# Kernel tuning notes

Hardware: AMD Instinct MI355X
Metric: run time of the kernel (lower is better)

Reference implementation:

```python
import jax, jax.numpy as jnp
import numpy as np

BITS = 4
MAXQ = (1 << BITS) - 1
PACK = 32 // BITS  # values packed per int32
GROUP_SIZE = 128


def dequant_weight(qweight, qzeros, scales, g_idx):
    """GPTQ tritonv2-style dequant: W[i,j] = (w_int[i,j] - z_int[g_idx[i],j]) * scales[g_idx[i],j]."""
    in_features = qweight.shape[0] * PACK
    out_features = qweight.shape[1]
    rows = jnp.arange(in_features)
    # unpack along infeatures: row i lives in qweight[i//PACK], nibble (i%PACK)
    w_int = (qweight[rows // PACK] >> ((rows % PACK) * BITS)[:, None]) & MAXQ  # [in, out]
    cols = jnp.arange(out_features)
    # unpack zeros along outfeatures
    z_int = (qzeros[:, cols // PACK] >> ((cols % PACK) * BITS)[None, :]) & MAXQ  # [groups, out]
    dt = scales.dtype
    return (w_int.astype(dt) - z_int.astype(dt)[g_idx]) * scales[g_idx]  # [in, out]


def setup_inputs() -> dict:
    key = jax.random.key(0)
    k1, k2, k3, k4, k5 = jax.random.split(key, 5)
    B, S, IN, OUT = 4, 2048, 4096, 11008
    groups = IN // GROUP_SIZE
    x = jax.random.normal(k1, (B, S, IN), dtype=jnp.float32)
    qweight = jax.random.randint(k2, (IN // PACK, OUT), 0, 2147483647, dtype=jnp.int32)
    qzeros = jax.random.randint(k3, (groups, OUT // PACK), 0, 2147483647, dtype=jnp.int32)
    scales = jax.random.uniform(k4, (groups, OUT), dtype=jnp.float32, minval=0.001, maxval=0.02)
    g_idx = (jnp.arange(IN) // GROUP_SIZE).astype(jnp.int32)
    bias = jax.random.normal(k5, (OUT,), dtype=jnp.float32) * 0.01
    return {"x": x, "qweight": qweight, "qzeros": qzeros, "scales": scales, "g_idx": g_idx, "bias": bias}


def reference(x, qweight, qzeros, scales, g_idx, bias):
    W = dequant_weight(qweight, qzeros, scales, g_idx)  # [in, out]
    out = x.reshape(-1, x.shape[-1]) @ W + bias  # [tokens, out]
    return out.reshape(x.shape[:-1] + (W.shape[1],)).astype(x.dtype)
```

## Files before the change

kernel.cpp:

```cpp
#include <hip/hip_runtime.h>

typedef __bf16 bf16x8 __attribute__((ext_vector_type(8)));
typedef __bf16 bf16x4 __attribute__((ext_vector_type(4)));
typedef float  f32x4  __attribute__((ext_vector_type(4)));

constexpr int BM  = 128;
constexpr int BN  = 128;
constexpr int BK  = 64;
constexpr int LDK = 72;

__global__ __launch_bounds__(256, 2)
void gptq_gemm_fused(const float* __restrict__ X,
                     const unsigned int* __restrict__ QW,
                     const unsigned int* __restrict__ QZ,
                     const float* __restrict__ SC,
                     const float* __restrict__ BIAS,
                     float* __restrict__ OUT,
                     const int M, const int N, const int K)
{
    __shared__ __bf16 As[BM * LDK];
    __shared__ __bf16 Bs[BN * LDK];

    const int tid = threadIdx.x;
    const int nTn = N / BN;
    const int m0  = (blockIdx.x / nTn) * BM;
    const int n0  = (blockIdx.x % nTn) * BN;

    const int lane = tid & 63;
    const int wave = tid >> 6;
    const int wm   = (wave >> 1) * 64;
    const int wn   = (wave & 1) * 64;
    const int l15  = lane & 15;
    const int lk8  = (lane >> 4) * 8;

    const int a_kc = (tid & 15) * 4;
    const int a_r0 = tid >> 4;
    const int b_c  = tid & 127;
    const int b_r0 = tid >> 7;
    const int N8   = N >> 3;

    f32x4 acc[4][4] = {};

    float4 av[8];
    unsigned int bw[4];
    float scale, nzs;

    auto load_tile = [&](int kt_) {
        const int k0 = kt_ * BK;
        #pragma unroll
        for (int i = 0; i < 8; ++i)
            av[i] = *(const float4*)&X[(m0 + a_r0 + 16 * i) * K + k0 + a_kc];
        const int qr = k0 >> 3;
        #pragma unroll
        for (int i = 0; i < 4; ++i)
            bw[i] = QW[(qr + b_r0 + 2 * i) * N + n0 + b_c];
        const int g = k0 >> 7;
        scale = SC[g * N + n0 + b_c];
        const unsigned int qzv = QZ[g * N8 + ((n0 + b_c) >> 3)];
        const int z = (qzv >> (((n0 + b_c) & 7) * 4)) & 15;
        nzs = (float)z * scale;
    };

    load_tile(0);

    const int kTiles = K / BK;
    for (int kt = 0; kt < kTiles; ++kt) {
        __syncthreads();

        #pragma unroll
        for (int i = 0; i < 8; ++i) {
            bf16x4 v = { (__bf16)av[i].x, (__bf16)av[i].y,
                         (__bf16)av[i].z, (__bf16)av[i].w };
            *(bf16x4*)&As[(a_r0 + 16 * i) * LDK + a_kc] = v;
        }
        {
            const float s = scale, nz = nzs;
            #pragma unroll
            for (int i = 0; i < 4; ++i) {
                const unsigned int w32 = bw[i];
                bf16x8 v;
                #pragma unroll
                for (int j = 0; j < 8; ++j) {
                    const int w = (w32 >> (4 * j)) & 15;
                    v[j] = (__bf16)((float)w * s - nz);
                }
                *(bf16x8*)&Bs[b_c * LDK + (b_r0 + 2 * i) * 8] = v;
            }
        }
        __syncthreads();

        if (kt + 1 < kTiles) load_tile(kt + 1);

        #pragma unroll
        for (int ks = 0; ks < 2; ++ks) {
            bf16x8 af[4], bfr[4];
            #pragma unroll
            for (int mi = 0; mi < 4; ++mi)
                af[mi] = *(bf16x8*)&As[(wm + mi * 16 + l15) * LDK + ks * 32 + lk8];
            #pragma unroll
            for (int ni = 0; ni < 4; ++ni)
                bfr[ni] = *(bf16x8*)&Bs[(wn + ni * 16 + l15) * LDK + ks * 32 + lk8];
            #pragma unroll
            for (int mi = 0; mi < 4; ++mi)
                #pragma unroll
                for (int ni = 0; ni < 4; ++ni)
                    acc[mi][ni] = __builtin_amdgcn_mfma_f32_16x16x32_bf16(
                        af[mi], bfr[ni], acc[mi][ni], 0, 0, 0);
        }
    }

    const int cb = n0 + wn + l15;
    const int rb = m0 + wm + (lane >> 4) * 4;
    #pragma unroll
    for (int ni = 0; ni < 4; ++ni) {
        const float bv = BIAS[cb + ni * 16];
        #pragma unroll
        for (int mi = 0; mi < 4; ++mi) {
            #pragma unroll
            for (int r = 0; r < 4; ++r)
                OUT[(size_t)(rb + mi * 16 + r) * N + cb + ni * 16] = acc[mi][ni][r] + bv;
        }
    }
}

extern "C" void kernel_launch(void* const* d_in, const int* in_sizes, int n_in,
                              void* d_out, int out_size, void* d_ws, size_t ws_size,
                              hipStream_t stream) {
    const float*        x    = (const float*)d_in[0];
    const unsigned int* qw   = (const unsigned int*)d_in[1];
    const unsigned int* qz   = (const unsigned int*)d_in[2];
    const float*        sc   = (const float*)d_in[3];
    const float*        bias = (const float*)d_in[5];
    float*              out  = (float*)d_out;

    const int K = in_sizes[4];
    const int N = in_sizes[5];
    const int M = in_sizes[0] / K;

    const dim3 grid((M / BM) * (N / BN));
    gptq_gemm_fused<<<grid, 256, 0, stream>>>(x, qw, qz, sc, bias, out, M, N, K);
}
```

Before: 1.373 ms.

## Split into bf16 pre-conversion, dequant-transpose, and async-LDS GEMM kernels

Replaces the single fused kernel with three kernels when workspace allows. The first converts X to bf16, the second dequantizes the weights into a transposed bf16 matrix through XOR-swizzled LDS, and the third is a GEMM that loads tiles directly into LDS with global_load_lds under a swizzled layout and a grouped block order. This removes the per-tile float-to-bf16 conversion and repeated dequantization from the GEMM inner loop, and halves the activation bytes the GEMM reads. The cost is extra workspace traffic to write and reread the bf16 X and W copies, and the GEMM still has no double buffering.

New measurement: 1.306 ms. -4.9%, faster.

```diff
diff --git a/kernel.cpp b/kernel.cpp
--- a/kernel.cpp
+++ b/kernel.cpp
@@ -3,6 +3,147 @@
 typedef __bf16 bf16x8 __attribute__((ext_vector_type(8)));
 typedef __bf16 bf16x4 __attribute__((ext_vector_type(4)));
 typedef float  f32x4  __attribute__((ext_vector_type(4)));
+
+typedef __attribute__((address_space(3))) unsigned int        lds_u32_t;
+typedef const __attribute__((address_space(1))) unsigned int  glob_u32_t;
+
+__global__ __launch_bounds__(256)
+void cvt_x_bf16(const float* __restrict__ X, __bf16* __restrict__ XB, long long n8)
+{
+    long long i = (long long)blockIdx.x * 256 + threadIdx.x;
+    if (i >= n8) return;
+    const float4* src = (const float4*)X + 2 * i;
+    float4 a = src[0], b = src[1];
+    bf16x8 v = { (__bf16)a.x, (__bf16)a.y, (__bf16)a.z, (__bf16)a.w,
+                 (__bf16)b.x, (__bf16)b.y, (__bf16)b.z, (__bf16)b.w };
+    *(bf16x8*)(XB + 8 * i) = v;
+}
+
+__global__ __launch_bounds__(256)
+void dequant_wt(const unsigned int* __restrict__ QW,
+                const unsigned int* __restrict__ QZ,
+                const float* __restrict__ SC,
+                __bf16* __restrict__ WT,
+                const int N, const int K)
+{
+    __shared__ __bf16 T[256 * 64];
+    const int tid = threadIdx.x;
+    const int nK  = K >> 6;
+    const int n0  = (blockIdx.x / nK) * 256;
+    const int k0  = (blockIdx.x % nK) * 64;
+
+    const int n = n0 + tid;
+    const int g = k0 >> 7;
+    const float s = SC[g * N + n];
+    const unsigned int qzv = QZ[g * (N >> 3) + (n >> 3)];
+    const float nz = (float)((qzv >> ((n & 7) * 4)) & 15) * s;
+    const int qr0 = k0 >> 3;
+
+    #pragma unroll
+    for (int i = 0; i < 8; ++i) {
+        const unsigned int w32 = QW[(size_t)(qr0 + i) * N + n];
+        bf16x8 v;
+        #pragma unroll
+        for (int j = 0; j < 8; ++j)
+            v[j] = (__bf16)((float)((w32 >> (4 * j)) & 15) * s - nz);
+        *(bf16x8*)((char*)T + tid * 128 + ((i ^ (tid & 7)) << 4)) = v;
+    }
+    __syncthreads();
+    #pragma unroll
+    for (int it = 0; it < 8; ++it) {
+        const int r = it * 32 + (tid >> 3);
+        const int c = tid & 7;
+        bf16x8 v = *(bf16x8*)((char*)T + r * 128 + ((c ^ (r & 7)) << 4));
+        *(bf16x8*)(WT + (size_t)(n0 + r) * K + k0 + c * 8) = v;
+    }
+}
+
+__global__ __launch_bounds__(256, 2)
+void gemm_bt_bf16(const __bf16* __restrict__ A,
+                  const __bf16* __restrict__ B,
+                  const float* __restrict__ BIAS,
+                  float* __restrict__ OUT,
+                  const int M, const int N, const int K)
+{
+    __shared__ __bf16 As[128 * 64];
+    __shared__ __bf16 Bs[128 * 64];
+
+    const int tid  = threadIdx.x;
+    const int lane = tid & 63;
+    const int wave = tid >> 6;
+
+    const int cpx = gridDim.x >> 3;
+    int bid = blockIdx.x;
+    bid = (bid & 7) * cpx + (bid >> 3);
+
+    const int nTn = N >> 7;
+    const int m0  = (bid / nTn) << 7;
+    const int n0  = (bid % nTn) << 7;
+
+    const int wm  = (wave >> 1) * 64;
+    const int wn  = (wave & 1) * 64;
+    const int l15 = lane & 15;
+    const int lhi = lane >> 4;
+
+    f32x4 acc[4][4] = {};
+
+    const size_t abase = (size_t)m0 * K;
+    const size_t bbase = (size_t)n0 * K;
+
+    const int kTiles = K >> 6;
+    for (int kt = 0; kt < kTiles; ++kt) {
+        const int k0 = kt << 6;
+        __syncthreads();
+        #pragma unroll
+        for (int i = 0; i < 4; ++i) {
+            const int c   = tid + 256 * i;
+            const int row = c >> 3;
+            const int sc_ = (c & 7) ^ (row & 7);
+            __builtin_amdgcn_global_load_lds(
+                (glob_u32_t*)(A + abase + (size_t)row * K + k0 + sc_ * 8),
+                (lds_u32_t*)((char*)As + c * 16), 16, 0, 0);
+            __builtin_amdgcn_global_load_lds(
+                (glob_u32_t*)(B + bbase + (size_t)row * K + k0 + sc_ * 8),
+                (lds_u32_t*)((char*)Bs + c * 16), 16, 0, 0);
+        }
+        __syncthreads();
+
+        #pragma unroll
+        for (int ks = 0; ks < 2; ++ks) {
+            bf16x8 af[4], bfr[4];
+            #pragma unroll
+            for (int mi = 0; mi < 4; ++mi) {
+                const int row = wm + mi * 16 + l15;
+                const int ch  = (ks * 4 + lhi) ^ (row & 7);
+                af[mi] = *(bf16x8*)((char*)As + row * 128 + (ch << 4));
+            }
+            #pragma unroll
+            for (int ni = 0; ni < 4; ++ni) {
+                const int row = wn + ni * 16 + l15;
+                const int ch  = (ks * 4 + lhi) ^ (row & 7);
+                bfr[ni] = *(bf16x8*)((char*)Bs + row * 128 + (ch << 4));
+            }
+            #pragma unroll
+            for (int mi = 0; mi < 4; ++mi)
+                #pragma unroll
+                for (int ni = 0; ni < 4; ++ni)
+                    acc[mi][ni] = __builtin_amdgcn_mfma_f32_16x16x32_bf16(
+                        af[mi], bfr[ni], acc[mi][ni], 0, 0, 0);
+        }
+    }
+
+    const int cb = n0 + wn + l15;
+    const int rb = m0 + wm + (lane >> 4) * 4;
+    #pragma unroll
+    for (int ni = 0; ni < 4; ++ni) {
+        const float bv = BIAS[cb + ni * 16];
+        #pragma unroll
+        for (int mi = 0; mi < 4; ++mi)
+            #pragma unroll
+            for (int r = 0; r < 4; ++r)
+                OUT[(size_t)(rb + mi * 16 + r) * N + cb + ni * 16] = acc[mi][ni][r] + bv;
+    }
+}
 
 constexpr int BM  = 128;
 constexpr int BN  = 128;
@@ -40,7 +181,6 @@
     const int N8   = N >> 3;
 
     f32x4 acc[4][4] = {};
-
     float4 av[8];
     unsigned int bw[4];
     float scale, nzs;
@@ -66,7 +206,6 @@
     const int kTiles = K / BK;
     for (int kt = 0; kt < kTiles; ++kt) {
         __syncthreads();
-
         #pragma unroll
         for (int i = 0; i < 8; ++i) {
             bf16x4 v = { (__bf16)av[i].x, (__bf16)av[i].y,
@@ -115,11 +254,10 @@
     for (int ni = 0; ni < 4; ++ni) {
         const float bv = BIAS[cb + ni * 16];
         #pragma unroll
-        for (int mi = 0; mi < 4; ++mi) {
+        for (int mi = 0; mi < 4; ++mi)
             #pragma unroll
             for (int r = 0; r < 4; ++r)
                 OUT[(size_t)(rb + mi * 16 + r) * N + cb + ni * 16] = acc[mi][ni][r] + bv;
-        }
     }
 }
 
@@ -137,6 +275,21 @@
     const int N = in_sizes[5];
     const int M = in_sizes[0] / K;
 
-    const dim3 grid((M / BM) * (N / BN));
-    gptq_gemm_fused<<<grid, 256, 0, stream>>>(x, qw, qz, sc, bias, out, M, N, K);
-}
+    const size_t needA = (size_t)M * K * 2;
+    const size_t needB = (size_t)N * K * 2;
+    const int    nwg   = (M / 128) * (N / 128);
+    const bool canSplit = (ws_size >= needA + needB) &&
+                          (M % 128 == 0) && (N % 256 == 0) && (K % 128 == 0) &&
+                          ((nwg & 7) == 0);
+
+    if (canSplit) {
+        __bf16* xb = (__bf16*)d_ws;
+        __bf16* wt = (__bf16*)((char*)d_ws + needA);
+        const long long n8 = (long long)M * K / 8;
+        cvt_x_bf16<<<(int)((n8 + 255) / 256), 256, 0, stream>>>(x, xb, n8);
+        dequant_wt<<<(N / 256) * (K / 64), 256, 0, stream>>>(qw, qz, sc, wt, N, K);
+        gemm_bt_bf16<<<nwg, 256, 0, stream>>>(xb, wt, bias, out, M, N, K);
+    } else {
+        gptq_gemm_fused<<<nwg, 256, 0, stream>>>(x, qw, qz, sc, bias, out, M, N, K);
+    }
+}
```
